# Performance work log

Measured on AMD Instinct MI355X. Metric: run time of the kernel, lower is better.

Reference implementation:

```python
import jax
import jax.numpy as jnp
import numpy as np
from jax import lax

B, L, A, C = 32, 128, 64, 128  # batch, length, n_agents, channels (in == out)
KT = 3                          # temporal kernel size, padding (KT-1)//2 keeps length


def setup_inputs() -> dict:
    key = jax.random.key(0)
    k1, k2, k3 = jax.random.split(key, 3)
    x = jax.random.normal(k1, (B, L, A, C), dtype=jnp.float32)
    # Conv2d weight [out_ch, in_ch, kt, 1] and bias, kaiming-ish scale
    W = jax.random.normal(k2, (C, C, KT, 1), dtype=jnp.float32) * (1.0 / np.sqrt(C * KT))
    b = jax.random.normal(k3, (C,), dtype=jnp.float32) * 0.01
    return {"x": x, "W": W, "b": b}


def reference(x, W, b):
    # x: [B, L, A, C] -> [B, C, L, A] (torch NCHW layout with H=time, W=agents)
    length, n_agents = x.shape[1], x.shape[2]
    xc = jnp.transpose(x, (0, 3, 1, 2))
    res = xc  # residual is identity (input_dim == output_dim, t_stride == 1)
    pad_t = (KT - 1) // 2
    y = lax.conv_general_dilated(
        xc, W,
        window_strides=(1, 1),
        padding=[(pad_t, pad_t), (0, 0)],
        dimension_numbers=("NCHW", "OIHW", "NCHW"),
    ) + b[None, :, None, None]  # [B, C, L, A]
    # Dense graph g[t,a,t',a'] = 1 iff t==t' or a==a'.  einsum('ncv,vw->ncw', x, g)
    # is exactly: sum over same time (all agents) + sum over same agent (all times) - self.
    agent_sum = jnp.sum(y, axis=3, keepdims=True)  # [B, C, L, 1]
    time_sum = jnp.sum(y, axis=2, keepdims=True)   # [B, C, 1, A]
    scale = (length + n_agents - 2) ** 0.5
    g = (agent_sum + time_sum - y) / scale
    out = jax.nn.relu(g + res)
    return jnp.transpose(out, (0, 2, 3, 1))  # [B, L, A, C]
```

## Files before the change

### kernel.cpp

```cpp
#include <hip/hip_runtime.h>
#include <stdint.h>


typedef __attribute__((ext_vector_type(8))) short bf16x8;
typedef __attribute__((ext_vector_type(4))) float f32x4;

__device__ __forceinline__ uint32_t f2bf(float f) {
    union { float f; uint32_t u; } v; v.f = f;
    return (v.u + 0x7FFFu + ((v.u >> 16) & 1u)) >> 16;
}
__device__ __forceinline__ float bf2f(uint32_t h) {
    union { uint32_t u; float f; } v; v.u = h << 16; return v.f;
}
__device__ __forceinline__ uint32_t pk2(float lo, float hi) {
    return f2bf(lo) | (f2bf(hi) << 16);
}
__device__ __forceinline__ void gll16(const void* g, void* l) {
    __builtin_amdgcn_global_load_lds((const __attribute__((address_space(1))) void*)g,
                                     (__attribute__((address_space(3))) void*)l, 16, 0, 0);
}

__global__ __launch_bounds__(256) void prep_kernel(
    const float* __restrict__ x, uint16_t* __restrict__ x16, uint16_t* __restrict__ xa16,
    const float* __restrict__ W, uint16_t* __restrict__ wp)
{
    const int tid = threadIdx.x;
    const int bid = blockIdx.x;
    if (bid >= 4160) {
        int o = (bid - 4160) * 256 + tid;
        int i = o & 7, lane = (o >> 3) & 63, nt = (o >> 9) & 7, ks = (o >> 12) & 3, d = o >> 14;
        int ci = ks * 32 + (lane >> 4) * 8 + i;
        int co = nt * 16 + (lane & 15);
        wp[o] = (uint16_t)f2bf(W[(co * 128 + ci) * 3 + d]);
        return;
    }
    const int b = bid / 130, tp = bid - b * 130;
    uint16_t* xo = x16 + (size_t)bid * 8192;
    if (tp == 0 || tp == 129) {
        const uint4 z = make_uint4(0, 0, 0, 0);
        #pragma unroll
        for (int k = 0; k < 4; ++k) *(uint4*)(xo + tid * 32 + k * 8) = z;
        if (tid < 16) *(uint4*)(xa16 + (size_t)bid * 128 + tid * 8) = z;
        return;
    }
    const int t = tp - 1;
    const int ci8 = (tid & 15) * 8, ag = tid >> 4;
    const float* xr = x + (size_t)(b * 128 + t) * 8192;
    float s[8];
    #pragma unroll
    for (int j = 0; j < 8; ++j) s[j] = 0.f;
    #pragma unroll
    for (int r = 0; r < 4; ++r) {
        const int a = ag * 4 + r;
        const float4 v0 = *(const float4*)(xr + a * 128 + ci8);
        const float4 v1 = *(const float4*)(xr + a * 128 + ci8 + 4);
        s[0] += v0.x; s[1] += v0.y; s[2] += v0.z; s[3] += v0.w;
        s[4] += v1.x; s[5] += v1.y; s[6] += v1.z; s[7] += v1.w;
        uint4 p;
        p.x = pk2(v0.x, v0.y); p.y = pk2(v0.z, v0.w);
        p.z = pk2(v1.x, v1.y); p.w = pk2(v1.z, v1.w);
        *(uint4*)(xo + a * 128 + ci8) = p;
    }
    __shared__ float red[16][128];
    *(float4*)&red[ag][ci8]     = make_float4(s[0], s[1], s[2], s[3]);
    *(float4*)&red[ag][ci8 + 4] = make_float4(s[4], s[5], s[6], s[7]);
    __syncthreads();
    if (tid < 128) {
        float v = 0.f;
        #pragma unroll
        for (int i = 0; i < 16; ++i) v += red[i][tid];
        xa16[(size_t)bid * 128 + tid] = (uint16_t)f2bf(v);
    }
}

__global__ __launch_bounds__(256) void xt_kernel(
    const uint16_t* __restrict__ x16, float* __restrict__ xt)
{
    const int tid = threadIdx.x, bid = blockIdx.x;
    const int a = bid & 63, b = bid >> 6;
    const int ci8 = (tid & 15) * 8, tg = tid >> 4;
    const uint16_t* base = x16 + ((size_t)(b * 130 + 1 + tg) * 64 + a) * 128 + ci8;
    float s[8];
    #pragma unroll
    for (int j = 0; j < 8; ++j) s[j] = 0.f;
    #pragma unroll
    for (int r = 0; r < 8; ++r) {
        const uint4 v = *(const uint4*)(base + (size_t)r * 16 * 8192);
        s[0] += bf2f(v.x & 0xFFFFu); s[1] += bf2f(v.x >> 16);
        s[2] += bf2f(v.y & 0xFFFFu); s[3] += bf2f(v.y >> 16);
        s[4] += bf2f(v.z & 0xFFFFu); s[5] += bf2f(v.z >> 16);
        s[6] += bf2f(v.w & 0xFFFFu); s[7] += bf2f(v.w >> 16);
    }
    __shared__ float red[16][128];
    *(float4*)&red[tg][ci8]     = make_float4(s[0], s[1], s[2], s[3]);
    *(float4*)&red[tg][ci8 + 4] = make_float4(s[4], s[5], s[6], s[7]);
    __syncthreads();
    if (tid < 128) {
        float v = 0.f;
        #pragma unroll
        for (int i = 0; i < 16; ++i) v += red[i][tid];
        xt[(size_t)bid * 128 + tid] = v;
    }
}

__global__ __launch_bounds__(256, 2) void sums_kernel(
    const uint16_t* __restrict__ xa16, const float* __restrict__ xt,
    const uint16_t* __restrict__ x16, const uint16_t* __restrict__ wp,
    const float* __restrict__ bias, float* __restrict__ asum, float* __restrict__ tsum)
{
    __shared__ __align__(16) uint16_t slab[130 * 128];
    const int tid = threadIdx.x;
    const int lane = tid & 63, wid = tid >> 6;
    const int wm = wid >> 1, wn = wid & 1;
    const int lr = lane & 15, lg = lane >> 4;
    f32x4 acc[4][4];
    #pragma unroll
    for (int mi = 0; mi < 4; ++mi)
        #pragma unroll
        for (int ni = 0; ni < 4; ++ni) acc[mi][ni] = (f32x4)0.f;

    if (blockIdx.x < 32) {
        const int b = blockIdx.x;
        #pragma unroll
        for (int it = 0; it < 9; ++it) {
            const int gg = it * 256 + tid;
            if (gg < 2080) {
                const int row = gg >> 4, sp = gg & 15;
                const int sl = sp ^ (row & 7);
                *(uint4*)(slab + gg * 8) =
                    *(const uint4*)(xa16 + (size_t)(b * 130 + row) * 128 + sl * 8);
            }
        }
        __syncthreads();
        #pragma unroll
        for (int g = 0; g < 4; ++g)
            #pragma unroll
            for (int d = 0; d < 3; ++d) {
                bf16x8 bq[4], af[4];
                #pragma unroll
                for (int ni = 0; ni < 4; ++ni)
                    bq[ni] = *(const bf16x8*)(wp + (size_t)((((d * 4 + g) * 8) + wn * 4 + ni) * 64 + lane) * 8);
                #pragma unroll
                for (int mi = 0; mi < 4; ++mi) {
                    const int row = wm * 64 + mi * 16 + lr + d;
                    af[mi] = *(const bf16x8*)(slab + row * 128 + ((g * 4 + lg) ^ (row & 7)) * 8);
                }
                #pragma unroll
                for (int mi = 0; mi < 4; ++mi)
                    #pragma unroll
                    for (int ni = 0; ni < 4; ++ni)
                        acc[mi][ni] = __builtin_amdgcn_mfma_f32_16x16x32_bf16(af[mi], bq[ni], acc[mi][ni], 0, 0, 0);
            }
        #pragma unroll
        for (int ni = 0; ni < 4; ++ni) {
            const int col = wn * 64 + ni * 16 + lr;
            const float bv = 64.f * bias[col];
            #pragma unroll
            for (int mi = 0; mi < 4; ++mi)
                #pragma unroll
                for (int j = 0; j < 4; ++j) {
                    const int t = wm * 64 + mi * 16 + lg * 4 + j;
                    asum[((size_t)b * 128 + t) * 128 + col] = acc[mi][ni][j] + bv;
                }
        }
        return;
    }

    const int bid = blockIdx.x - 32;
    const int r = tid >> 1, h = tid & 1;
    const int grow = bid * 128 + r, sb = grow >> 6, sa = grow & 63;
    #pragma unroll
    for (int d = 0; d < 3; ++d) {
        {
            const float* Sp = xt + (size_t)grow * 128 + h * 64;
            const uint16_t* Ep = x16 + ((size_t)(sb * 130 + (d == 0 ? 128 : 1)) * 64 + sa) * 128 + h * 64;
            #pragma unroll
            for (int k = 0; k < 8; ++k) {
                float4 f0 = *(const float4*)(Sp + k * 8);
                float4 f1 = *(const float4*)(Sp + k * 8 + 4);
                if (d != 1) {
                    const uint4 e = *(const uint4*)(Ep + k * 8);
                    f0.x -= bf2f(e.x & 0xFFFFu); f0.y -= bf2f(e.x >> 16);
                    f0.z -= bf2f(e.y & 0xFFFFu); f0.w -= bf2f(e.y >> 16);
                    f1.x -= bf2f(e.z & 0xFFFFu); f1.y -= bf2f(e.z >> 16);
                    f1.z -= bf2f(e.w & 0xFFFFu); f1.w -= bf2f(e.w >> 16);
                }
                uint4 o;
                o.x = pk2(f0.x, f0.y); o.y = pk2(f0.z, f0.w);
                o.z = pk2(f1.x, f1.y); o.w = pk2(f1.z, f1.w);
                const int sl = h * 8 + k;
                *(uint4*)(slab + r * 128 + (sl ^ (r & 7)) * 8) = o;
            }
        }
        __syncthreads();
        #pragma unroll
        for (int g = 0; g < 4; ++g) {
            bf16x8 bq[4], af[4];
            #pragma unroll
            for (int ni = 0; ni < 4; ++ni)
                bq[ni] = *(const bf16x8*)(wp + (size_t)((((d * 4 + g) * 8) + wn * 4 + ni) * 64 + lane) * 8);
            #pragma unroll
            for (int mi = 0; mi < 4; ++mi) {
                const int row = wm * 64 + mi * 16 + lr;
                af[mi] = *(const bf16x8*)(slab + row * 128 + ((g * 4 + lg) ^ (row & 7)) * 8);
            }
            #pragma unroll
            for (int mi = 0; mi < 4; ++mi)
                #pragma unroll
                for (int ni = 0; ni < 4; ++ni)
                    acc[mi][ni] = __builtin_amdgcn_mfma_f32_16x16x32_bf16(af[mi], bq[ni], acc[mi][ni], 0, 0, 0);
        }
        __syncthreads();
    }
    #pragma unroll
    for (int ni = 0; ni < 4; ++ni) {
        const int col = wn * 64 + ni * 16 + lr;
        const float bv = 128.f * bias[col];
        #pragma unroll
        for (int mi = 0; mi < 4; ++mi)
            #pragma unroll
            for (int j = 0; j < 4; ++j) {
                const int rg = bid * 128 + wm * 64 + mi * 16 + lg * 4 + j;
                tsum[(size_t)rg * 128 + col] = acc[mi][ni][j] + bv;
            }
    }
}

__global__ __launch_bounds__(512, 8) void conv_kernel(
    const uint16_t* __restrict__ x16, const uint16_t* __restrict__ wp,
    const float* __restrict__ bias, const float* __restrict__ asum,
    const float* __restrict__ tsum, float* __restrict__ out)
{
    __shared__ __align__(16) uint16_t slab[192 * 64];
    const int tid = threadIdx.x;
    const int raw = blockIdx.x;
    const int bid = (raw & 7) * 512 + (raw >> 3);
    const int b = bid >> 7, t = bid & 127;
    const int lane = tid & 63, wid = tid >> 6;
    const int lr = lane & 15, lg = lane >> 4;

    f32x4 acc[4];
    #pragma unroll
    for (int mi = 0; mi < 4; ++mi) acc[mi] = (f32x4)0.f;

#define STAGE(c) do {                                                          \
    _Pragma("unroll")                                                          \
    for (int k = 0; k < 3; ++k) {                                              \
        const int row = wid * 24 + k * 8 + (lane >> 3);                        \
        const int gran = (lane & 7) ^ (row & 7);                               \
        const uint16_t* src = x16 +                                            \
            ((size_t)((b * 130 + t + (row >> 6)) * 64 + (row & 63))) * 128 +   \
            (c) * 64 + gran * 8;                                               \
        gll16(src, slab + wid * 1536 + k * 512);                               \
    } } while (0)

#define MFMA_CHUNK(c) do {                                                     \
    _Pragma("unroll")                                                          \
    for (int d = 0; d < 3; ++d)                                                \
        _Pragma("unroll")                                                      \
        for (int g2 = 0; g2 < 2; ++g2) {                                       \
            const int ks = (c) * 2 + g2;                                       \
            bf16x8 bq, af[4];                                                  \
            bq = *(const bf16x8*)(wp +                                         \
                (size_t)((((d * 4 + ks) * 8) + wid) * 64 + lane) * 8);         \
            _Pragma("unroll")                                                  \
            for (int mi = 0; mi < 4; ++mi) {                                   \
                const int row = d * 64 + mi * 16 + lr;                         \
                af[mi] = *(const bf16x8*)(slab + row * 64 +                    \
                    (((g2 * 4 + lg) ^ (row & 7)) * 8));                        \
            }                                                                  \
            _Pragma("unroll")                                                  \
            for (int mi = 0; mi < 4; ++mi)                                     \
                acc[mi] = __builtin_amdgcn_mfma_f32_16x16x32_bf16(             \
                    af[mi], bq, acc[mi], 0, 0, 0);                             \
        } } while (0)

    STAGE(0);
    __syncthreads();
    MFMA_CHUNK(0);
    __syncthreads();
    STAGE(1);
    __syncthreads();
    MFMA_CHUNK(1);
    __syncthreads();

#undef STAGE
#undef MFMA_CHUNK

    {
        const int col = wid * 16 + lr;
        const float bv = bias[col];
        const int cl = col & 63;
        const int rbase = (col >> 6) << 7;
        #pragma unroll
        for (int mi = 0; mi < 4; ++mi)
            #pragma unroll
            for (int j = 0; j < 4; ++j) {
                const int a = mi * 16 + lg * 4 + j;
                slab[(rbase + a) * 64 + (cl ^ ((a & 7) << 3))] = (uint16_t)f2bf(acc[mi][j] + bv);
            }
    }
    __syncthreads();

    {
        const float inv = 0.07254762501100116f;
        const int cg = tid & 15, rb = tid >> 4;
        const float* ap = asum + ((size_t)(b * 128 + t)) * 128 + cg * 8;
        const float4 as0 = *(const float4*)ap, as1 = *(const float4*)(ap + 4);
        const float av[8] = {as0.x, as0.y, as0.z, as0.w, as1.x, as1.y, as1.z, as1.w};
        const int cl8 = (cg & 7) * 8;
        #pragma unroll
        for (int j = 0; j < 2; ++j) {
            const int a = j * 32 + rb;
            const int swz = cl8 ^ ((a & 7) << 3);
            uint4 yv, xv;
            if (cg < 8) {
                yv = *(const uint4*)(slab + a * 64 + swz);
                xv = *(const uint4*)(x16 + ((size_t)((b * 130 + t + 1) * 64 + a)) * 128 + cg * 8);
            } else {
                yv = *(const uint4*)(slab + (128 + a) * 64 + swz);
                xv = *(const uint4*)(slab + (64 + a) * 64 + swz);
            }
            const float* tp = tsum + ((size_t)(b * 64 + a)) * 128 + cg * 8;
            const float4 ts0 = *(const float4*)tp, ts1 = *(const float4*)(tp + 4);
            float yy[8], xx[8];
            yy[0] = bf2f(yv.x & 0xFFFFu); yy[1] = bf2f(yv.x >> 16);
            yy[2] = bf2f(yv.y & 0xFFFFu); yy[3] = bf2f(yv.y >> 16);
            yy[4] = bf2f(yv.z & 0xFFFFu); yy[5] = bf2f(yv.z >> 16);
            yy[6] = bf2f(yv.w & 0xFFFFu); yy[7] = bf2f(yv.w >> 16);
            xx[0] = bf2f(xv.x & 0xFFFFu); xx[1] = bf2f(xv.x >> 16);
            xx[2] = bf2f(xv.y & 0xFFFFu); xx[3] = bf2f(xv.y >> 16);
            xx[4] = bf2f(xv.z & 0xFFFFu); xx[5] = bf2f(xv.z >> 16);
            xx[6] = bf2f(xv.w & 0xFFFFu); xx[7] = bf2f(xv.w >> 16);
            const float tv[8] = {ts0.x, ts0.y, ts0.z, ts0.w, ts1.x, ts1.y, ts1.z, ts1.w};
            float o[8];
            #pragma unroll
            for (int i = 0; i < 8; ++i) {
                const float gg = (av[i] + tv[i] - yy[i]) * inv + xx[i];
                o[i] = gg > 0.f ? gg : 0.f;
            }
            float* op = out + ((size_t)((b * 128 + t) * 64 + a)) * 128 + cg * 8;
            *(float4*)op       = make_float4(o[0], o[1], o[2], o[3]);
            *(float4*)(op + 4) = make_float4(o[4], o[5], o[6], o[7]);
        }
    }
}

extern "C" void kernel_launch(void* const* d_in, const int* in_sizes, int n_in,
                              void* d_out, int out_size, void* d_ws, size_t ws_size,
                              hipStream_t stream) {
    const float* x    = (const float*)d_in[0];
    const float* W    = (const float*)d_in[1];
    const float* bias = (const float*)d_in[2];
    float* out = (float*)d_out;

    char* ws = (char*)d_ws;
    uint16_t* x16  = (uint16_t*)(ws);
    uint16_t* wp   = (uint16_t*)(ws + 68157440);
    uint16_t* xa16 = (uint16_t*)(ws + 68157440 + 98304);
    float* xt      = (float*)(ws + 68157440 + 98304 + 1064960);
    float* asum    = (float*)(ws + 68157440 + 98304 + 1064960 + 1048576);
    float* tsum    = (float*)(ws + 68157440 + 98304 + 1064960 + 1048576 + 2097152);

    prep_kernel <<<4352, 256, 0, stream>>>(x, x16, xa16, W, wp);
    xt_kernel   <<<2048, 256, 0, stream>>>(x16, xt);
    sums_kernel <<<48,   256, 0, stream>>>(xa16, xt, x16, wp, bias, asum, tsum);
    conv_kernel <<<4096, 512, 0, stream>>>(x16, wp, bias, asum, tsum, out);
}
```

Before: 115.7 us.

## Merge time-sum into prep kernel and double-buffer conv input slab

Folds the xt (per-agent time-sum) reduction into prep_kernel as extra blocks that read the fp32 input directly, which removes one kernel launch and its dependency on x16. In conv_kernel the LDS slab is doubled so the second channel chunk is staged while the first chunk's MFMAs run. The epilogue now takes the residual from the staged slab instead of reloading it from global memory. The larger LDS footprint lowers the occupancy bound from 8 to 6 blocks, and the fp32 reads in the new prep blocks move twice the bytes the bf16 path did.

Measured after the change: 129.7 us. +12.2%, slower.

```diff
diff --git a/kernel.cpp b/kernel.cpp
--- a/kernel.cpp
+++ b/kernel.cpp
@@ -22,10 +22,38 @@
 
 __global__ __launch_bounds__(256) void prep_kernel(
     const float* __restrict__ x, uint16_t* __restrict__ x16, uint16_t* __restrict__ xa16,
-    const float* __restrict__ W, uint16_t* __restrict__ wp)
+    const float* __restrict__ W, uint16_t* __restrict__ wp, float* __restrict__ xt)
 {
     const int tid = threadIdx.x;
     const int bid = blockIdx.x;
+    if (bid >= 4352) {
+        const int idx = bid - 4352;
+        const int a = idx & 63, b = idx >> 6;
+        const int ci8 = (tid & 15) * 8, tg = tid >> 4;
+        const float* base = x + ((size_t)(b * 128 + tg) * 64 + a) * 128 + ci8;
+        float s[8];
+        #pragma unroll
+        for (int j = 0; j < 8; ++j) s[j] = 0.f;
+        #pragma unroll
+        for (int r = 0; r < 8; ++r) {
+            const float* p = base + (size_t)r * 16 * 8192;
+            const float4 v0 = *(const float4*)p;
+            const float4 v1 = *(const float4*)(p + 4);
+            s[0] += v0.x; s[1] += v0.y; s[2] += v0.z; s[3] += v0.w;
+            s[4] += v1.x; s[5] += v1.y; s[6] += v1.z; s[7] += v1.w;
+        }
+        __shared__ float redx[16][128];
+        *(float4*)&redx[tg][ci8]     = make_float4(s[0], s[1], s[2], s[3]);
+        *(float4*)&redx[tg][ci8 + 4] = make_float4(s[4], s[5], s[6], s[7]);
+        __syncthreads();
+        if (tid < 128) {
+            float v = 0.f;
+            #pragma unroll
+            for (int i = 0; i < 16; ++i) v += redx[i][tid];
+            xt[(size_t)idx * 128 + tid] = v;
+        }
+        return;
+    }
     if (bid >= 4160) {
         int o = (bid - 4160) * 256 + tid;
         int i = o & 7, lane = (o >> 3) & 63, nt = (o >> 9) & 7, ks = (o >> 12) & 3, d = o >> 14;
@@ -70,36 +98,6 @@
         #pragma unroll
         for (int i = 0; i < 16; ++i) v += red[i][tid];
         xa16[(size_t)bid * 128 + tid] = (uint16_t)f2bf(v);
-    }
-}
-
-__global__ __launch_bounds__(256) void xt_kernel(
-    const uint16_t* __restrict__ x16, float* __restrict__ xt)
-{
-    const int tid = threadIdx.x, bid = blockIdx.x;
-    const int a = bid & 63, b = bid >> 6;
-    const int ci8 = (tid & 15) * 8, tg = tid >> 4;
-    const uint16_t* base = x16 + ((size_t)(b * 130 + 1 + tg) * 64 + a) * 128 + ci8;
-    float s[8];
-    #pragma unroll
-    for (int j = 0; j < 8; ++j) s[j] = 0.f;
-    #pragma unroll
-    for (int r = 0; r < 8; ++r) {
-        const uint4 v = *(const uint4*)(base + (size_t)r * 16 * 8192);
-        s[0] += bf2f(v.x & 0xFFFFu); s[1] += bf2f(v.x >> 16);
-        s[2] += bf2f(v.y & 0xFFFFu); s[3] += bf2f(v.y >> 16);
-        s[4] += bf2f(v.z & 0xFFFFu); s[5] += bf2f(v.z >> 16);
-        s[6] += bf2f(v.w & 0xFFFFu); s[7] += bf2f(v.w >> 16);
-    }
-    __shared__ float red[16][128];
-    *(float4*)&red[tg][ci8]     = make_float4(s[0], s[1], s[2], s[3]);
-    *(float4*)&red[tg][ci8 + 4] = make_float4(s[4], s[5], s[6], s[7]);
-    __syncthreads();
-    if (tid < 128) {
-        float v = 0.f;
-        #pragma unroll
-        for (int i = 0; i < 16; ++i) v += red[i][tid];
-        xt[(size_t)bid * 128 + tid] = v;
     }
 }
 
@@ -226,12 +224,12 @@
     }
 }
 
-__global__ __launch_bounds__(512, 8) void conv_kernel(
+__global__ __launch_bounds__(512, 6) void conv_kernel(
     const uint16_t* __restrict__ x16, const uint16_t* __restrict__ wp,
     const float* __restrict__ bias, const float* __restrict__ asum,
     const float* __restrict__ tsum, float* __restrict__ out)
 {
-    __shared__ __align__(16) uint16_t slab[192 * 64];
+    __shared__ __align__(16) uint16_t slab[2][192 * 64];
     const int tid = threadIdx.x;
     const int raw = blockIdx.x;
     const int bid = (raw & 7) * 512 + (raw >> 3);
@@ -251,7 +249,7 @@
         const uint16_t* src = x16 +                                            \
             ((size_t)((b * 130 + t + (row >> 6)) * 64 + (row & 63))) * 128 +   \
             (c) * 64 + gran * 8;                                               \
-        gll16(src, slab + wid * 1536 + k * 512);                               \
+        gll16(src, &slab[c][wid * 1536 + k * 512]);                            \
     } } while (0)
 
 #define MFMA_CHUNK(c) do {                                                     \
@@ -266,8 +264,8 @@
             _Pragma("unroll")                                                  \
             for (int mi = 0; mi < 4; ++mi) {                                   \
                 const int row = d * 64 + mi * 16 + lr;                         \
-                af[mi] = *(const bf16x8*)(slab + row * 64 +                    \
-                    (((g2 * 4 + lg) ^ (row & 7)) * 8));                        \
+                af[mi] = *(const bf16x8*)(&slab[c][row * 64 +                  \
+                    (((g2 * 4 + lg) ^ (row & 7)) * 8)]);                       \
             }                                                                  \
             _Pragma("unroll")                                                  \
             for (int mi = 0; mi < 4; ++mi)                                     \
@@ -277,9 +275,8 @@
 
     STAGE(0);
     __syncthreads();
+    STAGE(1);
     MFMA_CHUNK(0);
-    __syncthreads();
-    STAGE(1);
     __syncthreads();
     MFMA_CHUNK(1);
     __syncthreads();
@@ -290,14 +287,13 @@
     {
         const int col = wid * 16 + lr;
         const float bv = bias[col];
-        const int cl = col & 63;
-        const int rbase = (col >> 6) << 7;
+        const int cbuf = col >> 6, cl = col & 63;
         #pragma unroll
         for (int mi = 0; mi < 4; ++mi)
             #pragma unroll
             for (int j = 0; j < 4; ++j) {
                 const int a = mi * 16 + lg * 4 + j;
-                slab[(rbase + a) * 64 + (cl ^ ((a & 7) << 3))] = (uint16_t)f2bf(acc[mi][j] + bv);
+                slab[cbuf][a * 64 + (cl ^ ((a & 7) << 3))] = (uint16_t)f2bf(acc[mi][j] + bv);
             }
     }
     __syncthreads();
@@ -305,22 +301,16 @@
     {
         const float inv = 0.07254762501100116f;
         const int cg = tid & 15, rb = tid >> 4;
+        const int cbuf = cg >> 3, cl8 = (cg & 7) * 8;
         const float* ap = asum + ((size_t)(b * 128 + t)) * 128 + cg * 8;
         const float4 as0 = *(const float4*)ap, as1 = *(const float4*)(ap + 4);
         const float av[8] = {as0.x, as0.y, as0.z, as0.w, as1.x, as1.y, as1.z, as1.w};
-        const int cl8 = (cg & 7) * 8;
         #pragma unroll
         for (int j = 0; j < 2; ++j) {
             const int a = j * 32 + rb;
             const int swz = cl8 ^ ((a & 7) << 3);
-            uint4 yv, xv;
-            if (cg < 8) {
-                yv = *(const uint4*)(slab + a * 64 + swz);
-                xv = *(const uint4*)(x16 + ((size_t)((b * 130 + t + 1) * 64 + a)) * 128 + cg * 8);
-            } else {
-                yv = *(const uint4*)(slab + (128 + a) * 64 + swz);
-                xv = *(const uint4*)(slab + (64 + a) * 64 + swz);
-            }
+            const uint4 yv = *(const uint4*)(&slab[cbuf][a * 64 + swz]);
+            const uint4 xv = *(const uint4*)(&slab[cbuf][(64 + a) * 64 + swz]);
             const float* tp = tsum + ((size_t)(b * 64 + a)) * 128 + cg * 8;
             const float4 ts0 = *(const float4*)tp, ts1 = *(const float4*)(tp + 4);
             float yy[8], xx[8];
@@ -362,8 +352,7 @@
     float* asum    = (float*)(ws + 68157440 + 98304 + 1064960 + 1048576);
     float* tsum    = (float*)(ws + 68157440 + 98304 + 1064960 + 1048576 + 2097152);
 
-    prep_kernel <<<4352, 256, 0, stream>>>(x, x16, xa16, W, wp);
-    xt_kernel   <<<2048, 256, 0, stream>>>(x16, xt);
+    prep_kernel <<<6400, 256, 0, stream>>>(x, x16, xa16, W, wp, xt);
     sums_kernel <<<48,   256, 0, stream>>>(xa16, xt, x16, wp, bias, asum, tsum);
     conv_kernel <<<4096, 512, 0, stream>>>(x16, wp, bias, asum, tsum, out);
 }
```
